# Optimization experiments

Hardware: AMD Instinct MI355X
Metric: run time of the kernel (lower is better)

The kernel has to match this reference:

```python
import jax, jax.numpy as jnp
import numpy as np

N_USER = 100000
N_ITEM = 50000
N = N_USER + N_ITEM          # total graph nodes
D = 64                        # embed_size
NNZ = 4_000_000               # nonzeros in normalized adjacency
LAYERS = 3
B = 2048                      # batch_size
NEG = 4 * B                   # 4 negatives per positive (see create_bpr_loss)


def setup_inputs() -> dict:
    key = jax.random.key(0)
    ks = jax.random.split(key, 8)
    user_emb = jax.random.normal(ks[0], (N_USER, D), dtype=jnp.float32) * 0.1
    item_emb = jax.random.normal(ks[1], (N_ITEM, D), dtype=jnp.float32) * 0.1
    adj_row = jax.random.randint(ks[2], (NNZ,), 0, N, dtype=jnp.int32)
    adj_col = jax.random.randint(ks[3], (NNZ,), 0, N, dtype=jnp.int32)
    # symmetric-normalized adjacency values are small positive floats
    adj_val = jax.random.uniform(ks[4], (NNZ,), dtype=jnp.float32) * 0.05
    users = jax.random.randint(ks[5], (B,), 0, N_USER, dtype=jnp.int32)
    pos_items = jax.random.randint(ks[6], (B,), 0, N_ITEM, dtype=jnp.int32)
    neg_items = jax.random.randint(ks[7], (NEG,), 0, N_ITEM, dtype=jnp.int32)
    mask = jnp.zeros((1,), dtype=jnp.float32)      # unused in mode='plain'
    norm_adj = jnp.zeros((1,), dtype=jnp.float32)  # unused when attention=False
    return {
        "users": users, "pos_items": pos_items, "neg_items": neg_items,
        "mask": mask, "norm_adj": norm_adj,
        "user_emb": user_emb, "item_emb": item_emb,
        "adj_row": adj_row, "adj_col": adj_col, "adj_val": adj_val,
    }


def _spmm(row, col, val, x):
    """Sparse [N,N] @ dense [N,D] via gather + segment_sum."""
    gathered = val[:, None] * x[col]                      # [NNZ, D]
    return jax.ops.segment_sum(gathered, row, num_segments=N)


def reference(users, pos_items, neg_items, mask, norm_adj,
              user_emb, item_emb, adj_row, adj_col, adj_val):
    # ego embeddings for all nodes
    e0 = jnp.concatenate([user_emb, item_emb], axis=0)    # [N, D]
    # NOTE: the original torch code never updates ego_embeddings inside the
    # layer loop, so every layer appends the SAME A_hat @ E0. Hence:
    # light_out = mean([E0, A@E0, A@E0, ..., A@E0]) = (E0 + L*A@E0)/(L+1)
    ae0 = _spmm(adj_row, adj_col, adj_val, e0)            # [N, D]
    light_out = (e0 + LAYERS * ae0) / (LAYERS + 1)
    u_g = light_out[:N_USER]
    i_g = light_out[N_USER:]
    u_g_embeddings = u_g[users]
    pos_i_g_embeddings = i_g[pos_items]
    neg_i_g_embeddings = i_g[neg_items]
    return (u_g_embeddings, pos_i_g_embeddings, neg_i_g_embeddings)
```

## Files before the change

kernel.cpp:

```cpp
#include <hip/hip_runtime.h>

#define N_USER 100000
#define N_ITEM 50000
#define NTOT   150000
#define D      64
#define NNZ    4000000
#define B      2048
#define NEG    8192
#define NSLOT  (B + B + NEG)
#define CAP    128
#define NBW    ((NTOT + 31) / 32)

__device__ __forceinline__ int slot_row(int slot,
                                        const int* __restrict__ users,
                                        const int* __restrict__ pos,
                                        const int* __restrict__ neg) {
    if (slot < B)     return users[slot];
    if (slot < 2 * B) return N_USER + pos[slot - B];
    return N_USER + neg[slot - 2 * B];
}

__device__ __forceinline__ const float* e0_row(int c,
                                               const float* __restrict__ ue,
                                               const float* __restrict__ ie) {
    return (c < N_USER) ? &ue[(size_t)c * D] : &ie[(size_t)(c - N_USER) * D];
}

__global__ void k_clear(int* __restrict__ slotmap, unsigned int* __restrict__ bits) {
    int i = blockIdx.x * blockDim.x + threadIdx.x;
    if (i < NTOT) slotmap[i] = -1;
    if (i < NBW)  bits[i] = 0u;
}

__global__ void k_mark(const int* __restrict__ users,
                       const int* __restrict__ pos,
                       const int* __restrict__ neg,
                       int* __restrict__ slotmap,
                       unsigned int* __restrict__ bits,
                       int* __restrict__ cnt,
                       float* __restrict__ accd) {
    int slot = (blockIdx.x * blockDim.x + threadIdx.x) >> 6;
    int lane = threadIdx.x & 63;
    if (slot >= NSLOT) return;
    int r = slot_row(slot, users, pos, neg);
    int old = 0;
    if (lane == 0) old = atomicCAS(&slotmap[r], -1, slot);
    old = __shfl(old, 0);
    if (old == -1) {
        if (lane == 0) {
            cnt[slot] = 0;
            atomicOr(&bits[r >> 5], 1u << (r & 31));
        }
        accd[(size_t)slot * D + lane] = 0.0f;
    }
}

__global__ void k_scan(const int*   __restrict__ adj_row,
                       const int*   __restrict__ adj_col,
                       const float* __restrict__ adj_val,
                       const float* __restrict__ ue,
                       const float* __restrict__ ie,
                       const unsigned int* __restrict__ bits,
                       const int*   __restrict__ slotmap,
                       int*   __restrict__ cnt,
                       int2*  __restrict__ bcv,
                       float* __restrict__ accd) {
    __shared__ unsigned int sbits[NBW];
    {
        const int4* gb = (const int4*)bits;
        int4* sb = (int4*)sbits;
        for (int i = threadIdx.x; i < NBW / 4; i += blockDim.x) sb[i] = gb[i];
    }
    __syncthreads();

    int tid = blockIdx.x * blockDim.x + threadIdx.x;
    int nth = gridDim.x * blockDim.x;
    const int4*   row4 = (const int4*)adj_row;
    const int4*   col4 = (const int4*)adj_col;
    const float4* val4 = (const float4*)adj_val;

    for (int g = tid; g < NNZ / 4; g += nth) {
        int4   r = row4[g];
        int4   c = col4[g];
        float4 v = val4[g];
        #define PROC(RR, CC, VV)                                               \
        {                                                                      \
            unsigned int w = sbits[(RR) >> 5];                                 \
            if ((w >> ((RR) & 31)) & 1u) {                                     \
                int s = slotmap[RR];                                           \
                int idx = atomicAdd(&cnt[s], 1);                               \
                if (idx < CAP) {                                               \
                    bcv[s * CAP + idx] = make_int2(CC, __float_as_int(VV));    \
                } else {       \
                    const float* x = e0_row(CC, ue, ie);                       \
                    for (int d = 0; d < D; ++d)                                \
                        atomicAdd(&accd[(size_t)s * D + d], (VV) * x[d]);      \
                }                                                              \
            }                                                                  \
        }
        PROC(r.x, c.x, v.x)
        PROC(r.y, c.y, v.y)
        PROC(r.z, c.z, v.z)
        PROC(r.w, c.w, v.w)
        #undef PROC
    }
}

__global__ void k_rowacc(const int* __restrict__ users,
                         const int* __restrict__ pos,
                         const int* __restrict__ neg,
                         const int* __restrict__ slotmap,
                         const int* __restrict__ cnt,
                         const int2* __restrict__ bcv,
                         const float* __restrict__ ue,
                         const float* __restrict__ ie,
                         float* __restrict__ accd) {
    int slot = (blockIdx.x * blockDim.x + threadIdx.x) >> 6;
    int lane = threadIdx.x & 63;
    if (slot >= NSLOT) return;
    int r = slot_row(slot, users, pos, neg);
    if (slotmap[r] != slot) return;
    int n = cnt[slot];
    if (n > CAP) n = CAP;
    const int2* bb = &bcv[slot * CAP];
    float a = 0.0f;
    int i = 0;
    for (; i + 8 <= n; i += 8) {
        int2 p0 = bb[i],     p1 = bb[i + 1], p2 = bb[i + 2], p3 = bb[i + 3];
        int2 p4 = bb[i + 4], p5 = bb[i + 5], p6 = bb[i + 6], p7 = bb[i + 7];
        float x0 = e0_row(p0.x, ue, ie)[lane];
        float x1 = e0_row(p1.x, ue, ie)[lane];
        float x2 = e0_row(p2.x, ue, ie)[lane];
        float x3 = e0_row(p3.x, ue, ie)[lane];
        float x4 = e0_row(p4.x, ue, ie)[lane];
        float x5 = e0_row(p5.x, ue, ie)[lane];
        float x6 = e0_row(p6.x, ue, ie)[lane];
        float x7 = e0_row(p7.x, ue, ie)[lane];
        a += __int_as_float(p0.y) * x0;
        a += __int_as_float(p1.y) * x1;
        a += __int_as_float(p2.y) * x2;
        a += __int_as_float(p3.y) * x3;
        a += __int_as_float(p4.y) * x4;
        a += __int_as_float(p5.y) * x5;
        a += __int_as_float(p6.y) * x6;
        a += __int_as_float(p7.y) * x7;
    }
    for (; i < n; ++i) {
        int2 p = bb[i];
        a += __int_as_float(p.y) * e0_row(p.x, ue, ie)[lane];
    }
    accd[(size_t)slot * D + lane] += a;
}

__global__ void k_out(const int* __restrict__ users,
                      const int* __restrict__ pos,
                      const int* __restrict__ neg,
                      const float* __restrict__ ue,
                      const float* __restrict__ ie,
                      const int* __restrict__ slotmap,
                      const float* __restrict__ accd,
                      float* __restrict__ out) {
    int slot = (blockIdx.x * blockDim.x + threadIdx.x) >> 6;
    int lane = threadIdx.x & 63;
    if (slot >= NSLOT) return;
    int r = slot_row(slot, users, pos, neg);
    float e = (r < N_USER) ? ue[(size_t)r * D + lane]
                           : ie[(size_t)(r - N_USER) * D + lane];
    int id = slotmap[r];
    out[(size_t)slot * D + lane] = 0.25f * e + 0.75f * accd[(size_t)id * D + lane];
}

extern "C" void kernel_launch(void* const* d_in, const int* in_sizes, int n_in,
                              void* d_out, int out_size, void* d_ws, size_t ws_size,
                              hipStream_t stream) {
    const int*   users   = (const int*)  d_in[0];
    const int*   pos     = (const int*)  d_in[1];
    const int*   neg     = (const int*)  d_in[2];
    const float* ue      = (const float*)d_in[5];
    const float* ie      = (const float*)d_in[6];
    const int*   adj_row = (const int*)  d_in[7];
    const int*   adj_col = (const int*)  d_in[8];
    const float* adj_val = (const float*)d_in[9];
    float*       out     = (float*)      d_out;

    char* w = (char*)d_ws;
    int*          slotmap = (int*)w;          w += (size_t)NTOT * sizeof(int);
    unsigned int* bits    = (unsigned int*)w; w += (size_t)NBW * sizeof(unsigned int);
    int*          cnt     = (int*)w;          w += (size_t)NSLOT * sizeof(int);
    int2*         bcv     = (int2*)w;         w += (size_t)NSLOT * CAP * sizeof(int2);
    float*        accd    = (float*)w;

    k_clear <<<(NTOT + 255) / 256, 256, 0, stream>>>(slotmap, bits);
    k_mark  <<<(NSLOT * 64 + 255) / 256, 256, 0, stream>>>(users, pos, neg,
                                                           slotmap, bits, cnt, accd);
    k_scan  <<<2048, 256, 0, stream>>>(adj_row, adj_col, adj_val, ue, ie,
                                       bits, slotmap, cnt, bcv, accd);
    k_rowacc<<<(NSLOT * 64 + 255) / 256, 256, 0, stream>>>(users, pos, neg,
                                                           slotmap, cnt, bcv,
                                                           ue, ie, accd);
    k_out   <<<(NSLOT * 64 + 255) / 256, 256, 0, stream>>>(users, pos, neg, ue, ie,
                                                           slotmap, accd, out);
}
```

Before: 170.9 us.

## Drop slotmap clear, prefetch scan loads, vectorize row gather with float4

Claiming a slot now uses atomicOr on the bitmask, and the row-to-slot table is written only for winning rows, so the 150k-entry slotmap clear pass is gone. The scan kernel moves to 256 blocks of 1024 threads and software-prefetches the next int4/float4 chunk of row, col and val while it processes the current one. The row accumulation reads each neighbour's embedding as float4, with four 16-lane groups each handling a different neighbour, then combines them through xor shuffles. This trades a little extra shuffle and clamp logic for fewer memory transactions and a shorter init pass.

After: 163.2 us. 4.5% less time.

```diff
diff --git a/kernel.cpp b/kernel.cpp
--- a/kernel.cpp
+++ b/kernel.cpp
@@ -5,6 +5,7 @@
 #define NTOT   150000
 #define D      64
 #define NNZ    4000000
+#define NQ     (NNZ / 4)
 #define B      2048
 #define NEG    8192
 #define NSLOT  (B + B + NEG)
@@ -26,45 +27,44 @@
     return (c < N_USER) ? &ue[(size_t)c * D] : &ie[(size_t)(c - N_USER) * D];
 }
 
-__global__ void k_clear(int* __restrict__ slotmap, unsigned int* __restrict__ bits) {
+__global__ void k_clear(unsigned int* __restrict__ bits) {
     int i = blockIdx.x * blockDim.x + threadIdx.x;
-    if (i < NTOT) slotmap[i] = -1;
-    if (i < NBW)  bits[i] = 0u;
+    if (i < NBW) bits[i] = 0u;
 }
 
 __global__ void k_mark(const int* __restrict__ users,
                        const int* __restrict__ pos,
                        const int* __restrict__ neg,
-                       int* __restrict__ slotmap,
                        unsigned int* __restrict__ bits,
+                       int* __restrict__ rowslot,
                        int* __restrict__ cnt,
                        float* __restrict__ accd) {
     int slot = (blockIdx.x * blockDim.x + threadIdx.x) >> 6;
     int lane = threadIdx.x & 63;
     if (slot >= NSLOT) return;
     int r = slot_row(slot, users, pos, neg);
-    int old = 0;
-    if (lane == 0) old = atomicCAS(&slotmap[r], -1, slot);
-    old = __shfl(old, 0);
-    if (old == -1) {
-        if (lane == 0) {
-            cnt[slot] = 0;
-            atomicOr(&bits[r >> 5], 1u << (r & 31));
-        }
-        accd[(size_t)slot * D + lane] = 0.0f;
-    }
-}
-
-__global__ void k_scan(const int*   __restrict__ adj_row,
-                       const int*   __restrict__ adj_col,
-                       const float* __restrict__ adj_val,
-                       const float* __restrict__ ue,
-                       const float* __restrict__ ie,
-                       const unsigned int* __restrict__ bits,
-                       const int*   __restrict__ slotmap,
-                       int*   __restrict__ cnt,
-                       int2*  __restrict__ bcv,
-                       float* __restrict__ accd) {
+    int won = 0;
+    if (lane == 0) {
+        unsigned int bit = 1u << (r & 31);
+        unsigned int old = atomicOr(&bits[r >> 5], bit);
+        won = (old & bit) ? 0 : 1;
+        if (won) { rowslot[r] = slot; cnt[slot] = 0; }
+    }
+    won = __shfl(won, 0);
+    if (won) accd[(size_t)slot * D + lane] = 0.0f;
+}
+
+__global__ __launch_bounds__(1024)
+void k_scan(const int*   __restrict__ adj_row,
+            const int*   __restrict__ adj_col,
+            const float* __restrict__ adj_val,
+            const float* __restrict__ ue,
+            const float* __restrict__ ie,
+            const unsigned int* __restrict__ bits,
+            const int*   __restrict__ rowslot,
+            int*   __restrict__ cnt,
+            int2*  __restrict__ bcv,
+            float* __restrict__ accd) {
     __shared__ unsigned int sbits[NBW];
     {
         const int4* gb = (const int4*)bits;
@@ -79,37 +79,46 @@
     const int4*   col4 = (const int4*)adj_col;
     const float4* val4 = (const float4*)adj_val;
 
-    for (int g = tid; g < NNZ / 4; g += nth) {
-        int4   r = row4[g];
-        int4   c = col4[g];
-        float4 v = val4[g];
-        #define PROC(RR, CC, VV)                                               \
-        {                                                                      \
-            unsigned int w = sbits[(RR) >> 5];                                 \
-            if ((w >> ((RR) & 31)) & 1u) {                                     \
-                int s = slotmap[RR];                                           \
-                int idx = atomicAdd(&cnt[s], 1);                               \
-                if (idx < CAP) {                                               \
-                    bcv[s * CAP + idx] = make_int2(CC, __float_as_int(VV));    \
-                } else {       \
-                    const float* x = e0_row(CC, ue, ie);                       \
-                    for (int d = 0; d < D; ++d)                                \
-                        atomicAdd(&accd[(size_t)s * D + d], (VV) * x[d]);      \
-                }                                                              \
-            }                                                                  \
-        }
+    #define PROC(RR, CC, VV)                                               \
+    {                                                                      \
+        unsigned int w = sbits[(RR) >> 5];                                 \
+        if ((w >> ((RR) & 31)) & 1u) {                                     \
+            int s = rowslot[RR];                                           \
+            int idx = atomicAdd(&cnt[s], 1);                               \
+            if (idx < CAP) {                                               \
+                bcv[(size_t)s * CAP + idx] = make_int2(CC, __float_as_int(VV)); \
+            } else {       \
+                const float* x = e0_row(CC, ue, ie);                       \
+                for (int d = 0; d < D; ++d)                                \
+                    atomicAdd(&accd[(size_t)s * D + d], (VV) * x[d]);      \
+            }                                                              \
+        }                                                                  \
+    }
+
+    int g = tid;
+    if (g >= NQ) return;
+    int4   r = row4[g];
+    int4   c = col4[g];
+    float4 v = val4[g];
+    for (;;) {
+        int gn = g + nth;
+        bool more = gn < NQ;
+        int4 rn, cn; float4 vn;
+        if (more) { rn = row4[gn]; cn = col4[gn]; vn = val4[gn]; }
         PROC(r.x, c.x, v.x)
         PROC(r.y, c.y, v.y)
         PROC(r.z, c.z, v.z)
         PROC(r.w, c.w, v.w)
-        #undef PROC
-    }
+        if (!more) break;
+        g = gn; r = rn; c = cn; v = vn;
+    }
+    #undef PROC
 }
 
 __global__ void k_rowacc(const int* __restrict__ users,
                          const int* __restrict__ pos,
                          const int* __restrict__ neg,
-                         const int* __restrict__ slotmap,
+                         const int* __restrict__ rowslot,
                          const int* __restrict__ cnt,
                          const int2* __restrict__ bcv,
                          const float* __restrict__ ue,
@@ -119,37 +128,41 @@
     int lane = threadIdx.x & 63;
     if (slot >= NSLOT) return;
     int r = slot_row(slot, users, pos, neg);
-    if (slotmap[r] != slot) return;
+    if (rowslot[r] != slot) return;
     int n = cnt[slot];
     if (n > CAP) n = CAP;
-    const int2* bb = &bcv[slot * CAP];
-    float a = 0.0f;
-    int i = 0;
-    for (; i + 8 <= n; i += 8) {
-        int2 p0 = bb[i],     p1 = bb[i + 1], p2 = bb[i + 2], p3 = bb[i + 3];
-        int2 p4 = bb[i + 4], p5 = bb[i + 5], p6 = bb[i + 6], p7 = bb[i + 7];
-        float x0 = e0_row(p0.x, ue, ie)[lane];
-        float x1 = e0_row(p1.x, ue, ie)[lane];
-        float x2 = e0_row(p2.x, ue, ie)[lane];
-        float x3 = e0_row(p3.x, ue, ie)[lane];
-        float x4 = e0_row(p4.x, ue, ie)[lane];
-        float x5 = e0_row(p5.x, ue, ie)[lane];
-        float x6 = e0_row(p6.x, ue, ie)[lane];
-        float x7 = e0_row(p7.x, ue, ie)[lane];
-        a += __int_as_float(p0.y) * x0;
-        a += __int_as_float(p1.y) * x1;
-        a += __int_as_float(p2.y) * x2;
-        a += __int_as_float(p3.y) * x3;
-        a += __int_as_float(p4.y) * x4;
-        a += __int_as_float(p5.y) * x5;
-        a += __int_as_float(p6.y) * x6;
-        a += __int_as_float(p7.y) * x7;
-    }
-    for (; i < n; ++i) {
-        int2 p = bb[i];
-        a += __int_as_float(p.y) * e0_row(p.x, ue, ie)[lane];
-    }
-    accd[(size_t)slot * D + lane] += a;
+    const int2* bb = &bcv[(size_t)slot * CAP];
+    int sub = lane & 15, grp = lane >> 4;
+    float4 a = make_float4(0.f, 0.f, 0.f, 0.f);
+    for (int i = 0; i < n; i += 16) {
+        int m  = n - 1;
+        int e0 = i + grp, e1 = e0 + 4, e2 = e0 + 8, e3 = e0 + 12;
+        int2 p0 = bb[min(e0, m)];
+        int2 p1 = bb[min(e1, m)];
+        int2 p2 = bb[min(e2, m)];
+        int2 p3 = bb[min(e3, m)];
+        float4 x0 = ((const float4*)e0_row(p0.x, ue, ie))[sub];
+        float4 x1 = ((const float4*)e0_row(p1.x, ue, ie))[sub];
+        float4 x2 = ((const float4*)e0_row(p2.x, ue, ie))[sub];
+        float4 x3 = ((const float4*)e0_row(p3.x, ue, ie))[sub];
+        float v0 = (e0 < n) ? __int_as_float(p0.y) : 0.f;
+        float v1 = (e1 < n) ? __int_as_float(p1.y) : 0.f;
+        float v2 = (e2 < n) ? __int_as_float(p2.y) : 0.f;
+        float v3 = (e3 < n) ? __int_as_float(p3.y) : 0.f;
+        a.x += v0 * x0.x; a.y += v0 * x0.y; a.z += v0 * x0.z; a.w += v0 * x0.w;
+        a.x += v1 * x1.x; a.y += v1 * x1.y; a.z += v1 * x1.z; a.w += v1 * x1.w;
+        a.x += v2 * x2.x; a.y += v2 * x2.y; a.z += v2 * x2.z; a.w += v2 * x2.w;
+        a.x += v3 * x3.x; a.y += v3 * x3.y; a.z += v3 * x3.z; a.w += v3 * x3.w;
+    }
+    a.x += __shfl_xor(a.x, 16); a.y += __shfl_xor(a.y, 16);
+    a.z += __shfl_xor(a.z, 16); a.w += __shfl_xor(a.w, 16);
+    a.x += __shfl_xor(a.x, 32); a.y += __shfl_xor(a.y, 32);
+    a.z += __shfl_xor(a.z, 32); a.w += __shfl_xor(a.w, 32);
+    if (grp == 0) {
+        float4* dst = (float4*)&accd[(size_t)slot * D];
+        float4 o = dst[sub];
+        dst[sub] = make_float4(o.x + a.x, o.y + a.y, o.z + a.z, o.w + a.w);
+    }
 }
 
 __global__ void k_out(const int* __restrict__ users,
@@ -157,7 +170,7 @@
                       const int* __restrict__ neg,
                       const float* __restrict__ ue,
                       const float* __restrict__ ie,
-                      const int* __restrict__ slotmap,
+                      const int* __restrict__ rowslot,
                       const float* __restrict__ accd,
                       float* __restrict__ out) {
     int slot = (blockIdx.x * blockDim.x + threadIdx.x) >> 6;
@@ -166,7 +179,7 @@
     int r = slot_row(slot, users, pos, neg);
     float e = (r < N_USER) ? ue[(size_t)r * D + lane]
                            : ie[(size_t)(r - N_USER) * D + lane];
-    int id = slotmap[r];
+    int id = rowslot[r];
     out[(size_t)slot * D + lane] = 0.25f * e + 0.75f * accd[(size_t)id * D + lane];
 }
 
@@ -184,20 +197,20 @@
     float*       out     = (float*)      d_out;
 
     char* w = (char*)d_ws;
-    int*          slotmap = (int*)w;          w += (size_t)NTOT * sizeof(int);
+    int*          rowslot = (int*)w;          w += (size_t)NTOT * sizeof(int);
     unsigned int* bits    = (unsigned int*)w; w += (size_t)NBW * sizeof(unsigned int);
     int*          cnt     = (int*)w;          w += (size_t)NSLOT * sizeof(int);
     int2*         bcv     = (int2*)w;         w += (size_t)NSLOT * CAP * sizeof(int2);
     float*        accd    = (float*)w;
 
-    k_clear <<<(NTOT + 255) / 256, 256, 0, stream>>>(slotmap, bits);
+    k_clear <<<(NBW + 255) / 256, 256, 0, stream>>>(bits);
     k_mark  <<<(NSLOT * 64 + 255) / 256, 256, 0, stream>>>(users, pos, neg,
-                                                           slotmap, bits, cnt, accd);
-    k_scan  <<<2048, 256, 0, stream>>>(adj_row, adj_col, adj_val, ue, ie,
-                                       bits, slotmap, cnt, bcv, accd);
+                                                           bits, rowslot, cnt, accd);
+    k_scan  <<<256, 1024, 0, stream>>>(adj_row, adj_col, adj_val, ue, ie,
+                                       bits, rowslot, cnt, bcv, accd);
     k_rowacc<<<(NSLOT * 64 + 255) / 256, 256, 0, stream>>>(users, pos, neg,
-                                                           slotmap, cnt, bcv,
+                                                           rowslot, cnt, bcv,
                                                            ue, ie, accd);
     k_out   <<<(NSLOT * 64 + 255) / 256, 256, 0, stream>>>(users, pos, neg, ue, ie,
-                                                           slotmap, accd, out);
-}
+                                                           rowslot, accd, out);
+}
```
